# Kernel tuning notes

Measured on AMD Instinct MI355X. Metric: run time of the kernel, lower is better.

The kernel has to match this reference:

```python
import jax, jax.numpy as jnp
import numpy as np

N_QUBITS = 20
SUPPORT = (3, 8, 15)   # qubit_support
BATCH = 8
DIM = 2 ** len(SUPPORT)  # 8


def setup_inputs() -> dict:
    key = jax.random.key(0)
    ks = jax.random.split(key, 5)
    state_shape = (2,) * N_QUBITS + (BATCH,)
    state_real = jax.random.normal(ks[0], state_shape, dtype=jnp.float32)
    state_imag = jax.random.normal(ks[1], state_shape, dtype=jnp.float32)
    a = jax.random.normal(ks[2], (DIM, DIM), dtype=jnp.float32)
    b = jax.random.normal(ks[3], (DIM, DIM), dtype=jnp.float32)
    h_real = ((a + a.T) * 0.5)[..., None]   # (DIM, DIM, 1) symmetric
    h_imag = ((b - b.T) * 0.5)[..., None]   # antisymmetric -> H Hermitian
    t = jax.random.uniform(ks[4], (BATCH,), dtype=jnp.float32)
    return {"state_real": state_real, "state_imag": state_imag,
            "h_real": h_real, "h_imag": h_imag, "t": t}


def reference(state_real, state_imag, h_real, h_imag, t):
    # state: (2,)*N_QUBITS + (BATCH,) complex
    state = state_real + 1j * state_imag
    # Hermitian generator, hmat layout (d, d, batch_h=1) as in the module buffer
    H = (h_real + 1j * h_imag)[..., 0]                      # (DIM, DIM)
    # _unitary: expm(-1j * t * H) per batch. H Hermitian -> exact via eigh.
    w, V = jnp.linalg.eigh(H)                               # w real (DIM,), V (DIM, DIM)
    phases = jnp.exp(-1j * (t[:, None] * w[None, :]))       # (BATCH, DIM)
    U = jnp.einsum('ik,bk,jk->bij', V, phases, V.conj())    # (BATCH, DIM, DIM)
    # apply_operator: reshape U into per-qubit indices and contract at SUPPORT axes
    s = len(SUPPORT)
    op = U.reshape((BATCH,) + (2,) * (2 * s))               # (B, out bits..., in bits...)
    B_LBL = 100
    out_lbls = [200 + i for i in range(s)]
    op_axes = [B_LBL] + out_lbls + list(SUPPORT)
    state_axes = list(range(N_QUBITS)) + [B_LBL]
    out_axes = list(range(N_QUBITS))
    for i, q in enumerate(SUPPORT):
        out_axes[q] = out_lbls[i]
    out_axes = out_axes + [B_LBL]
    return jnp.einsum(op, op_axes, state, state_axes, out_axes)
```

## Files before the change

kernel.cpp:

```cpp
#include <hip/hip_runtime.h>
#include <hip/hip_bf16.h>


__global__ void expm_kernel(const float* __restrict__ h_real,
                            const float* __restrict__ h_imag,
                            const float* __restrict__ t,
                            float2* __restrict__ U) {
    __shared__ double Mre[8][9], Mim[8][9];
    __shared__ double Tre[8][9], Tim[8][9];
    __shared__ double Ere[8][9], Eim[8][9];

    const int b   = blockIdx.x;
    const int tid = threadIdx.x;
    const int o   = tid >> 3;
    const int i   = tid & 7;

    const double tb  = (double)t[b];
    const double hre = (double)h_real[o * 8 + i];
    const double him = (double)h_imag[o * 8 + i];

    const double scale = 1.0 / 64.0;
    const double mre = tb * him * scale;
    const double mim = -tb * hre * scale;

    Mre[o][i] = mre; Mim[o][i] = mim;
    Tre[o][i] = mre; Tim[o][i] = mim;
    double ere = ((o == i) ? 1.0 : 0.0) + mre;
    double eim = mim;
    __syncthreads();

    for (int k = 2; k <= 12; ++k) {
        double sre = 0.0, sim = 0.0;
        #pragma unroll
        for (int j = 0; j < 8; ++j) {
            sre += Tre[o][j] * Mre[j][i] - Tim[o][j] * Mim[j][i];
            sim += Tre[o][j] * Mim[j][i] + Tim[o][j] * Mre[j][i];
        }
        const double inv = 1.0 / (double)k;
        sre *= inv; sim *= inv;
        __syncthreads();
        Tre[o][i] = sre; Tim[o][i] = sim;
        ere += sre; eim += sim;
        __syncthreads();
    }

    Ere[o][i] = ere; Eim[o][i] = eim;
    __syncthreads();

    for (int sq = 0; sq < 6; ++sq) {
        double sre = 0.0, sim = 0.0;
        #pragma unroll
        for (int j = 0; j < 8; ++j) {
            sre += Ere[o][j] * Ere[j][i] - Eim[o][j] * Eim[j][i];
            sim += Ere[o][j] * Eim[j][i] + Eim[o][j] * Ere[j][i];
        }
        __syncthreads();
        Ere[o][i] = sre; Eim[o][i] = sim;
        __syncthreads();
    }

    U[b * 64 + tid] = make_float2((float)Ere[o][i], (float)Eim[o][i]);
}

__global__ __launch_bounds__(256) void apply_kernel(
        const float* __restrict__ sre_g,
        const float* __restrict__ sim_g,
        const float2* __restrict__ U,
        float* __restrict__ out)
{
    __shared__ alignas(16) float2 uLds[8 * 66];
    const int tid = threadIdx.x;
    for (int v = tid; v < 512; v += 256) {
        uLds[(v >> 6) * 66 + (v & 63)] = U[v];
    }
    __syncthreads();

    const int r = blockIdx.x * 256 + tid;
    const int b = r & 7;

    unsigned addr = (r & 0x7Fu)
                  | ((r & 0x1F80u)  << 1)
                  | ((r & 0x1E000u) << 2)
                  | ((r & 0xE0000u) << 3);

    float xre[8], xim[8];
    #pragma unroll
    for (int i = 0; i < 8; ++i) {
        const unsigned off = addr + ((i & 4) ? 524288u : 0u)
                                  + ((i & 2) ? 16384u  : 0u)
                                  + ((i & 1) ? 128u    : 0u);
        xre[i] = sre_g[off];
        xim[i] = sim_g[off];
    }

    const float4* urow = reinterpret_cast<const float4*>(uLds) + b * 33;

    #pragma unroll
    for (int o = 0; o < 8; ++o) {
        float are = 0.f;
        #pragma unroll
        for (int p = 0; p < 4; ++p) {
            const float4 u = urow[o * 4 + p];
            const int i0 = 2 * p, i1 = 2 * p + 1;
            are += u.x * xre[i0] - u.y * xim[i0];
            are += u.z * xre[i1] - u.w * xim[i1];
        }
        const unsigned off = addr + ((o & 4) ? 524288u : 0u)
                                  + ((o & 2) ? 16384u  : 0u)
                                  + ((o & 1) ? 128u    : 0u);
        out[off] = are;
    }
}

extern "C" void kernel_launch(void* const* d_in, const int* in_sizes, int n_in,
                              void* d_out, int out_size, void* d_ws, size_t ws_size,
                              hipStream_t stream) {
    const float* state_real = (const float*)d_in[0];
    const float* state_imag = (const float*)d_in[1];
    const float* h_real     = (const float*)d_in[2];
    const float* h_imag     = (const float*)d_in[3];
    const float* t          = (const float*)d_in[4];

    float2* U = (float2*)d_ws;

    expm_kernel<<<8, 64, 0, stream>>>(h_real, h_imag, t, U);

    apply_kernel<<<4096, 256, 0, stream>>>(state_real, state_imag, U,
                                           (float*)d_out);
}
```

Measured before the change: 28.66 us.

## Fuse matrix exponential into apply kernel with float4 vectorized state access

Merges the separate expm and apply kernels into one launch. Every block now recomputes the 8 batch unitaries in fp32 (Taylor order 10, 5 squarings) in shared memory, which removes a kernel launch and the round trip of U through global memory. Each thread handles four consecutive batch elements with float4 loads and stores, so the grid shrinks to a quarter of the blocks. The cost is redundant expm work in each of 1024 blocks, more shared memory per block, and lower precision than the previous fp64 exponential.

```diff
diff --git a/kernel.cpp b/kernel.cpp
--- a/kernel.cpp
+++ b/kernel.cpp
@@ -1,114 +1,125 @@
 #include <hip/hip_runtime.h>
-#include <hip/hip_bf16.h>
 
 
-__global__ void expm_kernel(const float* __restrict__ h_real,
-                            const float* __restrict__ h_imag,
-                            const float* __restrict__ t,
-                            float2* __restrict__ U) {
-    __shared__ double Mre[8][9], Mim[8][9];
-    __shared__ double Tre[8][9], Tim[8][9];
-    __shared__ double Ere[8][9], Eim[8][9];
+#define SUP_OFF(m) ( ((m)&4 ? 524288u : 0u) + ((m)&2 ? 16384u : 0u) + ((m)&1 ? 128u : 0u) )
 
-    const int b   = blockIdx.x;
+__global__ __launch_bounds__(256, 4) void fused_evolve_kernel(
+        const float* __restrict__ sre_g,
+        const float* __restrict__ sim_g,
+        const float* __restrict__ h_real,
+        const float* __restrict__ h_imag,
+        const float* __restrict__ t_g,
+        float* __restrict__ out)
+{
+    __shared__ float Tre[8][64], Tim[8][64];
+    __shared__ float Mre[8][64], Mim[8][64];
+    __shared__ float Ere[8][64], Eim[8][64];
+    __shared__ alignas(16) float Upre[512];
+    __shared__ alignas(16) float Upim[512];
+
     const int tid = threadIdx.x;
-    const int o   = tid >> 3;
-    const int i   = tid & 7;
 
-    const double tb  = (double)t[b];
-    const double hre = (double)h_real[o * 8 + i];
-    const double him = (double)h_imag[o * 8 + i];
+    {
+        const int b  = tid >> 5;
+        const int e0 = tid & 31;
+        const int e1 = e0 + 32;
+        const int o0 = e0 >> 3, i0 = e0 & 7;
+        const int o1 = e1 >> 3, i1 = e1 & 7;
 
-    const double scale = 1.0 / 64.0;
-    const double mre = tb * him * scale;
-    const double mim = -tb * hre * scale;
+        const float sc = t_g[b] * (1.0f / 32.0f);
+        const float m0re =  sc * h_imag[e0];
+        const float m0im = -sc * h_real[e0];
+        const float m1re =  sc * h_imag[e1];
+        const float m1im = -sc * h_real[e1];
 
-    Mre[o][i] = mre; Mim[o][i] = mim;
-    Tre[o][i] = mre; Tim[o][i] = mim;
-    double ere = ((o == i) ? 1.0 : 0.0) + mre;
-    double eim = mim;
-    __syncthreads();
+        Mre[b][e0] = m0re; Mim[b][e0] = m0im;
+        Mre[b][e1] = m1re; Mim[b][e1] = m1im;
+        Tre[b][e0] = m0re; Tim[b][e0] = m0im;
+        Tre[b][e1] = m1re; Tim[b][e1] = m1im;
+        float a0re = (o0 == i0 ? 1.f : 0.f) + m0re, a0im = m0im;
+        float a1re = (o1 == i1 ? 1.f : 0.f) + m1re, a1im = m1im;
+        __syncthreads();
 
-    for (int k = 2; k <= 12; ++k) {
-        double sre = 0.0, sim = 0.0;
-        #pragma unroll
-        for (int j = 0; j < 8; ++j) {
-            sre += Tre[o][j] * Mre[j][i] - Tim[o][j] * Mim[j][i];
-            sim += Tre[o][j] * Mim[j][i] + Tim[o][j] * Mre[j][i];
+        for (int k = 2; k <= 10; ++k) {
+            float s0re = 0.f, s0im = 0.f, s1re = 0.f, s1im = 0.f;
+            #pragma unroll
+            for (int j = 0; j < 8; ++j) {
+                float tre = Tre[b][o0 * 8 + j], tim = Tim[b][o0 * 8 + j];
+                float mre = Mre[b][j * 8 + i0], mim = Mim[b][j * 8 + i0];
+                s0re += tre * mre - tim * mim;
+                s0im += tre * mim + tim * mre;
+                tre = Tre[b][o1 * 8 + j]; tim = Tim[b][o1 * 8 + j];
+                mre = Mre[b][j * 8 + i1]; mim = Mim[b][j * 8 + i1];
+                s1re += tre * mre - tim * mim;
+                s1im += tre * mim + tim * mre;
+            }
+            const float inv = 1.0f / (float)k;
+            s0re *= inv; s0im *= inv; s1re *= inv; s1im *= inv;
+            __syncthreads();
+            Tre[b][e0] = s0re; Tim[b][e0] = s0im;
+            Tre[b][e1] = s1re; Tim[b][e1] = s1im;
+            a0re += s0re; a0im += s0im;
+            a1re += s1re; a1im += s1im;
+            __syncthreads();
         }
-        const double inv = 1.0 / (double)k;
-        sre *= inv; sim *= inv;
+
+        Ere[b][e0] = a0re; Eim[b][e0] = a0im;
+        Ere[b][e1] = a1re; Eim[b][e1] = a1im;
         __syncthreads();
-        Tre[o][i] = sre; Tim[o][i] = sim;
-        ere += sre; eim += sim;
-        __syncthreads();
+
+        for (int sq = 0; sq < 5; ++sq) {
+            float s0re = 0.f, s0im = 0.f, s1re = 0.f, s1im = 0.f;
+            #pragma unroll
+            for (int j = 0; j < 8; ++j) {
+                float xre = Ere[b][o0 * 8 + j], xim = Eim[b][o0 * 8 + j];
+                float yre = Ere[b][j * 8 + i0], yim = Eim[b][j * 8 + i0];
+                s0re += xre * yre - xim * yim;
+                s0im += xre * yim + xim * yre;
+                xre = Ere[b][o1 * 8 + j]; xim = Eim[b][o1 * 8 + j];
+                yre = Ere[b][j * 8 + i1]; yim = Eim[b][j * 8 + i1];
+                s1re += xre * yre - xim * yim;
+                s1im += xre * yim + xim * yre;
+            }
+            __syncthreads();
+            if (sq < 4) {
+                Ere[b][e0] = s0re; Eim[b][e0] = s0im;
+                Ere[b][e1] = s1re; Eim[b][e1] = s1im;
+            } else {
+                Upre[e0 * 8 + b] = s0re; Upim[e0 * 8 + b] = s0im;
+                Upre[e1 * 8 + b] = s1re; Upim[e1 * 8 + b] = s1im;
+            }
+            __syncthreads();
+        }
     }
 
-    Ere[o][i] = ere; Eim[o][i] = eim;
-    __syncthreads();
+    const int r0 = (blockIdx.x * 256 + tid) << 2;
+    unsigned addr = (r0 & 0x7Fu)
+                  | ((r0 & 0x1F80u)  << 1)
+                  | ((r0 & 0x1E000u) << 2)
+                  | ((r0 & 0xE0000u) << 3);
+    const int b0 = r0 & 7;
 
-    for (int sq = 0; sq < 6; ++sq) {
-        double sre = 0.0, sim = 0.0;
-        #pragma unroll
-        for (int j = 0; j < 8; ++j) {
-            sre += Ere[o][j] * Ere[j][i] - Eim[o][j] * Eim[j][i];
-            sim += Ere[o][j] * Eim[j][i] + Eim[o][j] * Ere[j][i];
-        }
-        __syncthreads();
-        Ere[o][i] = sre; Eim[o][i] = sim;
-        __syncthreads();
-    }
-
-    U[b * 64 + tid] = make_float2((float)Ere[o][i], (float)Eim[o][i]);
-}
-
-__global__ __launch_bounds__(256) void apply_kernel(
-        const float* __restrict__ sre_g,
-        const float* __restrict__ sim_g,
-        const float2* __restrict__ U,
-        float* __restrict__ out)
-{
-    __shared__ alignas(16) float2 uLds[8 * 66];
-    const int tid = threadIdx.x;
-    for (int v = tid; v < 512; v += 256) {
-        uLds[(v >> 6) * 66 + (v & 63)] = U[v];
-    }
-    __syncthreads();
-
-    const int r = blockIdx.x * 256 + tid;
-    const int b = r & 7;
-
-    unsigned addr = (r & 0x7Fu)
-                  | ((r & 0x1F80u)  << 1)
-                  | ((r & 0x1E000u) << 2)
-                  | ((r & 0xE0000u) << 3);
-
-    float xre[8], xim[8];
+    float4 xre[8], xim[8];
     #pragma unroll
     for (int i = 0; i < 8; ++i) {
-        const unsigned off = addr + ((i & 4) ? 524288u : 0u)
-                                  + ((i & 2) ? 16384u  : 0u)
-                                  + ((i & 1) ? 128u    : 0u);
-        xre[i] = sre_g[off];
-        xim[i] = sim_g[off];
+        const unsigned off = addr + SUP_OFF(i);
+        xre[i] = *(const float4*)(sre_g + off);
+        xim[i] = *(const float4*)(sim_g + off);
     }
-
-    const float4* urow = reinterpret_cast<const float4*>(uLds) + b * 33;
 
     #pragma unroll
     for (int o = 0; o < 8; ++o) {
-        float are = 0.f;
+        float4 a = make_float4(0.f, 0.f, 0.f, 0.f);
         #pragma unroll
-        for (int p = 0; p < 4; ++p) {
-            const float4 u = urow[o * 4 + p];
-            const int i0 = 2 * p, i1 = 2 * p + 1;
-            are += u.x * xre[i0] - u.y * xim[i0];
-            are += u.z * xre[i1] - u.w * xim[i1];
+        for (int i = 0; i < 8; ++i) {
+            const float4 ur = *(const float4*)&Upre[(o * 8 + i) * 8 + b0];
+            const float4 ui = *(const float4*)&Upim[(o * 8 + i) * 8 + b0];
+            a.x += ur.x * xre[i].x - ui.x * xim[i].x;
+            a.y += ur.y * xre[i].y - ui.y * xim[i].y;
+            a.z += ur.z * xre[i].z - ui.z * xim[i].z;
+            a.w += ur.w * xre[i].w - ui.w * xim[i].w;
         }
-        const unsigned off = addr + ((o & 4) ? 524288u : 0u)
-                                  + ((o & 2) ? 16384u  : 0u)
-                                  + ((o & 1) ? 128u    : 0u);
-        out[off] = are;
+        *(float4*)(out + addr + SUP_OFF(o)) = a;
     }
 }
 
@@ -121,10 +132,7 @@
     const float* h_imag     = (const float*)d_in[3];
     const float* t          = (const float*)d_in[4];
 
-    float2* U = (float2*)d_ws;
-
-    expm_kernel<<<8, 64, 0, stream>>>(h_real, h_imag, t, U);
-
-    apply_kernel<<<4096, 256, 0, stream>>>(state_real, state_imag, U,
-                                           (float*)d_out);
+    fused_evolve_kernel<<<1024, 256, 0, stream>>>(state_real, state_imag,
+                                                  h_real, h_imag, t,
+                                                  (float*)d_out);
 }
```

Result: no change. 28.86 us (+0.7%).

## Compute expm in fp32 with fewer terms, process four rows per thread

Applied to the files above, without the earlier changes.

The matrix-exponential kernel switches from double to float, uses a 1/32 scaling with 10 Taylor terms and 5 squarings, and writes U already transposed into the column layout the apply kernel needs. The apply kernel now has each thread handle four state rows. It streams the inputs column by column and accumulates outputs in registers, so each U column loaded from LDS is reused across four rows, and the grid drops to 1024 blocks. In exchange, register pressure rises, fp32 accuracy in expm is lower, and there are fewer blocks to hide memory latency.

```diff
diff --git a/kernel.cpp b/kernel.cpp
--- a/kernel.cpp
+++ b/kernel.cpp
@@ -1,114 +1,134 @@
 #include <hip/hip_runtime.h>
-#include <hip/hip_bf16.h>
 
+
+#define SUP_OFF(m) ( ((m)&4 ? 524288u : 0u) + ((m)&2 ? 16384u : 0u) + ((m)&1 ? 128u : 0u) )
 
 __global__ void expm_kernel(const float* __restrict__ h_real,
                             const float* __restrict__ h_imag,
-                            const float* __restrict__ t,
-                            float2* __restrict__ U) {
-    __shared__ double Mre[8][9], Mim[8][9];
-    __shared__ double Tre[8][9], Tim[8][9];
-    __shared__ double Ere[8][9], Eim[8][9];
+                            const float* __restrict__ t_g,
+                            float* __restrict__ U)
+{
+    __shared__ float Tre[64], Tim[64], Mre[64], Mim[64], Ere[64], Eim[64];
 
-    const int b   = blockIdx.x;
-    const int tid = threadIdx.x;
-    const int o   = tid >> 3;
-    const int i   = tid & 7;
+    const int b = blockIdx.x;
+    const int e = threadIdx.x;
+    const int o = e >> 3, i = e & 7;
 
-    const double tb  = (double)t[b];
-    const double hre = (double)h_real[o * 8 + i];
-    const double him = (double)h_imag[o * 8 + i];
+    const float sc  = t_g[b] * (1.0f / 32.0f);
+    const float mre =  sc * h_imag[e];
+    const float mim = -sc * h_real[e];
 
-    const double scale = 1.0 / 64.0;
-    const double mre = tb * him * scale;
-    const double mim = -tb * hre * scale;
-
-    Mre[o][i] = mre; Mim[o][i] = mim;
-    Tre[o][i] = mre; Tim[o][i] = mim;
-    double ere = ((o == i) ? 1.0 : 0.0) + mre;
-    double eim = mim;
+    Mre[e] = mre; Mim[e] = mim;
+    Tre[e] = mre; Tim[e] = mim;
+    float are = (o == i ? 1.f : 0.f) + mre;
+    float aim = mim;
     __syncthreads();
 
-    for (int k = 2; k <= 12; ++k) {
-        double sre = 0.0, sim = 0.0;
+    for (int k = 2; k <= 10; ++k) {
+        float sre = 0.f, sim = 0.f;
         #pragma unroll
         for (int j = 0; j < 8; ++j) {
-            sre += Tre[o][j] * Mre[j][i] - Tim[o][j] * Mim[j][i];
-            sim += Tre[o][j] * Mim[j][i] + Tim[o][j] * Mre[j][i];
+            const float tre = Tre[o * 8 + j], tim = Tim[o * 8 + j];
+            const float qre = Mre[j * 8 + i], qim = Mim[j * 8 + i];
+            sre += tre * qre - tim * qim;
+            sim += tre * qim + tim * qre;
         }
-        const double inv = 1.0 / (double)k;
+        const float inv = 1.0f / (float)k;
         sre *= inv; sim *= inv;
         __syncthreads();
-        Tre[o][i] = sre; Tim[o][i] = sim;
-        ere += sre; eim += sim;
+        Tre[e] = sre; Tim[e] = sim;
+        are += sre; aim += sim;
         __syncthreads();
     }
 
-    Ere[o][i] = ere; Eim[o][i] = eim;
+    Ere[e] = are; Eim[e] = aim;
     __syncthreads();
 
-    for (int sq = 0; sq < 6; ++sq) {
-        double sre = 0.0, sim = 0.0;
+    for (int sq = 0; sq < 5; ++sq) {
+        float sre = 0.f, sim = 0.f;
         #pragma unroll
         for (int j = 0; j < 8; ++j) {
-            sre += Ere[o][j] * Ere[j][i] - Eim[o][j] * Eim[j][i];
-            sim += Ere[o][j] * Eim[j][i] + Eim[o][j] * Ere[j][i];
+            const float xre = Ere[o * 8 + j], xim = Eim[o * 8 + j];
+            const float yre = Ere[j * 8 + i], yim = Eim[j * 8 + i];
+            sre += xre * yre - xim * yim;
+            sim += xre * yim + xim * yre;
         }
         __syncthreads();
-        Ere[o][i] = sre; Eim[o][i] = sim;
-        __syncthreads();
+        if (sq < 4) {
+            Ere[e] = sre; Eim[e] = sim;
+            __syncthreads();
+        } else {
+            U[(i * 8 + b) * 16 + 2 * o]     = sre;
+            U[(i * 8 + b) * 16 + 2 * o + 1] = sim;
+        }
     }
-
-    U[b * 64 + tid] = make_float2((float)Ere[o][i], (float)Eim[o][i]);
 }
 
-__global__ __launch_bounds__(256) void apply_kernel(
+__global__ __launch_bounds__(256, 4) void apply_kernel(
         const float* __restrict__ sre_g,
         const float* __restrict__ sim_g,
-        const float2* __restrict__ U,
+        const float4* __restrict__ U4,
         float* __restrict__ out)
 {
-    __shared__ alignas(16) float2 uLds[8 * 66];
+    __shared__ alignas(16) float uL[8 * 8 * 20];
     const int tid = threadIdx.x;
-    for (int v = tid; v < 512; v += 256) {
-        uLds[(v >> 6) * 66 + (v & 63)] = U[v];
+    {
+        const float4 u = U4[tid];
+        const int ib = tid >> 2, k = tid & 3;
+        *(float4*)&uL[ib * 20 + k * 4] = u;
     }
     __syncthreads();
 
-    const int r = blockIdx.x * 256 + tid;
-    const int b = r & 7;
+    const unsigned rbase = blockIdx.x * 1024u + tid;
+    const int b = tid & 7;
 
-    unsigned addr = (r & 0x7Fu)
-                  | ((r & 0x1F80u)  << 1)
-                  | ((r & 0x1E000u) << 2)
-                  | ((r & 0xE0000u) << 3);
+    unsigned addr[4];
+    #pragma unroll
+    for (int s = 0; s < 4; ++s) {
+        const unsigned r = rbase + 256u * s;
+        addr[s] = (r & 0x7Fu)
+                | ((r & 0x1F80u)  << 1)
+                | ((r & 0x1E000u) << 2)
+                | ((r & 0xE0000u) << 3);
+    }
 
-    float xre[8], xim[8];
+    float acc[4][8];
+    #pragma unroll
+    for (int s = 0; s < 4; ++s)
+        #pragma unroll
+        for (int o = 0; o < 8; ++o) acc[s][o] = 0.f;
+
     #pragma unroll
     for (int i = 0; i < 8; ++i) {
-        const unsigned off = addr + ((i & 4) ? 524288u : 0u)
-                                  + ((i & 2) ? 16384u  : 0u)
-                                  + ((i & 1) ? 128u    : 0u);
-        xre[i] = sre_g[off];
-        xim[i] = sim_g[off];
+        const float4* uv = (const float4*)&uL[(i * 8 + b) * 20];
+        const float4 u01 = uv[0];
+        const float4 u23 = uv[1];
+        const float4 u45 = uv[2];
+        const float4 u67 = uv[3];
+        const unsigned so = SUP_OFF(i);
+        #pragma unroll
+        for (int s = 0; s < 4; ++s) {
+            const unsigned off = addr[s] + so;
+            const float xr = sre_g[off];
+            const float xi = sim_g[off];
+            acc[s][0] += u01.x * xr - u01.y * xi;
+            acc[s][1] += u01.z * xr - u01.w * xi;
+            acc[s][2] += u23.x * xr - u23.y * xi;
+            acc[s][3] += u23.z * xr - u23.w * xi;
+            acc[s][4] += u45.x * xr - u45.y * xi;
+            acc[s][5] += u45.z * xr - u45.w * xi;
+            acc[s][6] += u67.x * xr - u67.y * xi;
+            acc[s][7] += u67.z * xr - u67.w * xi;
+        }
     }
-
-    const float4* urow = reinterpret_cast<const float4*>(uLds) + b * 33;
 
     #pragma unroll
     for (int o = 0; o < 8; ++o) {
-        float are = 0.f;
+        const unsigned so = SUP_OFF(o);
         #pragma unroll
-        for (int p = 0; p < 4; ++p) {
-            const float4 u = urow[o * 4 + p];
-            const int i0 = 2 * p, i1 = 2 * p + 1;
-            are += u.x * xre[i0] - u.y * xim[i0];
-            are += u.z * xre[i1] - u.w * xim[i1];
+        for (int s = 0; s < 4; ++s) {
+            out[addr[s] + so] = acc[s][o];
         }
-        const unsigned off = addr + ((o & 4) ? 524288u : 0u)
-                                  + ((o & 2) ? 16384u  : 0u)
-                                  + ((o & 1) ? 128u    : 0u);
-        out[off] = are;
     }
 }
 
@@ -121,10 +141,10 @@
     const float* h_imag     = (const float*)d_in[3];
     const float* t          = (const float*)d_in[4];
 
-    float2* U = (float2*)d_ws;
+    float* U = (float*)d_ws;
 
     expm_kernel<<<8, 64, 0, stream>>>(h_real, h_imag, t, U);
 
-    apply_kernel<<<4096, 256, 0, stream>>>(state_real, state_imag, U,
-                                           (float*)d_out);
+    apply_kernel<<<1024, 256, 0, stream>>>(state_real, state_imag,
+                                           (const float4*)U, (float*)d_out);
 }
```

New measurement: 28.08 us. -2.0%, faster.
